# Kernel tuning notes

Hardware: AMD Instinct MI355X
Metric: run time of the kernel (lower is better)

Reference implementation:

```python
import jax, jax.numpy as jnp
import numpy as np

T, B, OBS, H, P, L, A = 512, 128, 512, 256, 128, 4, 4


def _ln(x, scale, bias, eps=1e-6):
    mu = jnp.mean(x, axis=-1, keepdims=True)
    var = jnp.mean((x - mu) ** 2, axis=-1, keepdims=True)
    return (x - mu) * jax.lax.rsqrt(var + eps) * scale + bias


def _binop(qi, qj):
    # S5 reset-aware associative operator: elements (A, b, reset_flag)
    Ai, bi, ci = qi
    Aj, bj, cj = qj
    A = (Aj * Ai) * (1.0 - cj) + Aj * cj
    b = (Aj * bi + bj) * (1.0 - cj) + bj * cj
    c = ci * (1.0 - cj) + cj
    return A, b, c


def _s5_layer(x, dones, h0, scale, bias, lam_re, lam_im, b_re, b_im, c_re, c_im, d_vec, log_step, glu_W, glu_b):
    # x: (T,B,H) real, dones: (T,B), h0: (B,P) complex64
    skip = x
    u = _ln(x, scale, bias)                                  # prenorm
    lam = lam_re + 1j * lam_im                               # (P,)
    step = jnp.exp(log_step)                                 # (P,)
    lam_bar = jnp.exp(lam * step)                            # ZOH discretization
    B_bar = ((lam_bar - 1.0) / lam)[:, None] * (b_re + 1j * b_im)  # (P,H)
    Bu = jnp.einsum('tbh,ph->tbp', u.astype(jnp.complex64), B_bar)  # (T,B,P)
    A_el = jnp.concatenate([jnp.ones((1, B, P), jnp.complex64),
                            jnp.broadcast_to(lam_bar.astype(jnp.complex64), (T, B, P))], axis=0)
    b_el = jnp.concatenate([h0[None], Bu], axis=0)
    c_el = jnp.concatenate([jnp.zeros((1, B, 1), jnp.float32), dones[..., None]], axis=0)
    _, xs, _ = jax.lax.associative_scan(_binop, (A_el, b_el, c_el), axis=0)
    xs = xs[1:]                                              # (T,B,P) complex states
    new_h = xs[-1]
    C = c_re + 1j * c_im                                     # (H,P)
    ys = 2.0 * jnp.real(jnp.einsum('tbp,hp->tbh', xs, C)) + d_vec * u  # conj_sym output + D*u
    z = _ln(ys, scale, bias)                                 # gtrxl norm (shared LayerNorm params)
    z = jax.nn.gelu(z)                                       # half_glu1
    z = z * jax.nn.sigmoid(z @ glu_W + glu_b)
    return skip + z, new_h


def setup_inputs() -> dict:
    key = jax.random.key(0)
    ks = jax.random.split(key, 40)
    f32 = jnp.float32

    def n(i, shape, s=1.0):
        return jax.random.normal(ks[i], shape, f32) * s

    inp = {}
    inp['obs'] = n(0, (T, B, OBS))
    inp['dones'] = (jax.random.uniform(ks[1], (T, B)) < 0.01).astype(f32)
    inp['hidden_re'] = jnp.zeros((L, B, P), f32)
    inp['hidden_im'] = jnp.zeros((L, B, P), f32)
    inp['enc0_W'] = n(2, (OBS, 128), 1.0 / np.sqrt(OBS))
    inp['enc0_b'] = jnp.zeros((128,), f32)
    inp['enc1_W'] = n(3, (128, H), 1.0 / np.sqrt(128))
    inp['enc1_b'] = jnp.zeros((H,), f32)
    inp['norm_scale'] = jnp.ones((L, H), f32)
    inp['norm_bias'] = jnp.zeros((L, H), f32)
    inp['Lambda_re'] = -0.5 * jax.random.uniform(ks[4], (L, P), f32) - 0.1
    inp['Lambda_im'] = n(5, (L, P), np.pi)
    inp['B_re'] = n(6, (L, P, H), 1.0 / np.sqrt(H))
    inp['B_im'] = n(7, (L, P, H), 1.0 / np.sqrt(H))
    inp['C_re'] = n(8, (L, H, P), 1.0 / np.sqrt(2 * P))
    inp['C_im'] = n(9, (L, H, P), 1.0 / np.sqrt(2 * P))
    inp['D'] = n(10, (L, H))
    inp['log_step'] = jax.random.uniform(ks[11], (L, P), f32, np.log(1e-3), np.log(1e-1))
    inp['glu_W'] = n(12, (L, H, H), 1.0 / np.sqrt(H))
    inp['glu_b'] = jnp.zeros((L, H), f32)
    inp['ab0_W'] = n(13, (H, 128), 1.0 / np.sqrt(H))
    inp['ab0_b'] = jnp.zeros((128,), f32)
    inp['ab1_W'] = n(14, (128, 128), 1.0 / np.sqrt(128))
    inp['ab1_b'] = jnp.zeros((128,), f32)
    inp['adec_W'] = n(15, (128, A), 0.01 / np.sqrt(128))
    inp['adec_b'] = jnp.full((A,), 0.5, f32)
    inp['log_std'] = jnp.full((A,), -0.7, f32)
    inp['vb0_W'] = n(16, (H, 128), 1.0 / np.sqrt(H))
    inp['vb0_b'] = jnp.zeros((128,), f32)
    inp['vb1_W'] = n(17, (128, 128), 1.0 / np.sqrt(128))
    inp['vb1_b'] = jnp.zeros((128,), f32)
    inp['vdec_W'] = n(18, (128, 1), 1.0 / np.sqrt(128))
    inp['vdec_b'] = jnp.zeros((1,), f32)
    return inp


def reference(obs, dones, hidden_re, hidden_im, enc0_W, enc0_b, enc1_W, enc1_b,
              norm_scale, norm_bias, Lambda_re, Lambda_im, B_re, B_im, C_re, C_im,
              D, log_step, glu_W, glu_b, ab0_W, ab0_b, ab1_W, ab1_b, adec_W, adec_b,
              log_std, vb0_W, vb0_b, vb1_W, vb1_b, vdec_W, vdec_b):
    e = jax.nn.leaky_relu(obs @ enc0_W + enc0_b)
    e = jax.nn.leaky_relu(e @ enc1_W + enc1_b)
    h0 = (hidden_re + 1j * hidden_im).astype(jnp.complex64)  # (L,B,P)
    new_h = []
    for l in range(L):
        e, hl = _s5_layer(e, dones, h0[l], norm_scale[l], norm_bias[l],
                          Lambda_re[l], Lambda_im[l], B_re[l], B_im[l],
                          C_re[l], C_im[l], D[l], log_step[l], glu_W[l], glu_b[l])
        new_h.append(hl)
    new_h = jnp.stack(new_h)
    am = jax.nn.leaky_relu(e @ ab0_W + ab0_b)
    am = jax.nn.leaky_relu(am @ ab1_W + ab1_b)
    am = am @ adec_W + adec_b                                # actor mean (T,B,A)
    v = jax.nn.leaky_relu(e @ vb0_W + vb0_b)
    v = jax.nn.leaky_relu(v @ vb1_W + vb1_b)
    v = v @ vdec_W + vdec_b                                  # critic (T,B,1)
    sc = jnp.broadcast_to(jnp.exp(log_std), am.shape)        # Normal scale (pi params)
    out = jnp.concatenate([am, sc, v], axis=-1)              # (T,B,2A+1)
    return out, jnp.real(new_h), jnp.imag(new_h)
```

## Files before the change

kernel.cpp:

```cpp
#include <hip/hip_runtime.h>
#include <math.h>

#define TT 512
#define BB 128
#define OBSD 512
#define HD 256
#define PD 128
#define LD 4
#define NTB (TT*BB)

typedef __bf16 bf16x8 __attribute__((ext_vector_type(8)));
typedef float  f32x4  __attribute__((ext_vector_type(4)));

__device__ __forceinline__ float bf2f(unsigned short u) {
    return __uint_as_float(((unsigned)u) << 16);
}
__device__ __forceinline__ unsigned short f2bf(float f) {
    unsigned u = __float_as_uint(f);
    unsigned r = (u + 0x7FFFu + ((u >> 16) & 1u)) >> 16;
    return (unsigned short)r;
}
__device__ __forceinline__ float gelu_f(float x) {
    float x3 = x * x * x;
    return 0.5f * x * (1.f + tanhf(0.7978845608028654f * (x + 0.044715f * x3)));
}


template<int LAST>
__global__ __launch_bounds__(512) void layer_k(
    const unsigned short* __restrict__ XSp,
    const unsigned short* __restrict__ Uaux,
    const unsigned short* __restrict__ CT,
    const unsigned short* __restrict__ GT,
    const unsigned short* __restrict__ BT2,
    const float* __restrict__ Dv,
    const float* __restrict__ ns1, const float* __restrict__ nb1,
    const float* __restrict__ glub,
    const float* __restrict__ ns2, const float* __restrict__ nb2,
    unsigned short* __restrict__ Xio,
    unsigned short* __restrict__ Uo,
    unsigned short* __restrict__ BUo)
{
    const int N = 256;
    __shared__ unsigned short smA[2 * 2048];
    __shared__ unsigned short smB[2 * 8192];
    __shared__ unsigned short zbuf[64 * 264];
    float2 (*red)[8] = reinterpret_cast<float2(*)[8]>(&smA[0]);
    int tid = threadIdx.x;
    int lane = tid & 63, w = tid >> 6;
    int m16 = lane & 15, quad = lane >> 4;
    int m0 = blockIdx.x * 64;
    int colb = w * 32 + quad * 4;

    auto stage1 = [&](int slot, int kt) {
        int k0 = kt << 5;
#pragma unroll
        for (int j = 0; j < 2; ++j) {
            int e = (w * 2 + j) * 128 + lane * 2;
            int row = e >> 5, kb = e & 31;
            const unsigned short* g = XSp + (size_t)(m0 + row) * 256 + k0 + kb;
            __builtin_amdgcn_global_load_lds(
                (const __attribute__((address_space(1))) void*)g,
                (__attribute__((address_space(3))) void*)(smA + slot * 2048 + e), 4, 0, 0);
        }
#pragma unroll
        for (int j = 0; j < 2; ++j) {
            int e = (w * 2 + j) * 512 + lane * 8;
            int r = e >> 5, kq = e & 31;
            const unsigned short* g = CT + (size_t)r * 256 + k0 + kq;
            __builtin_amdgcn_global_load_lds(
                (const __attribute__((address_space(1))) void*)g,
                (__attribute__((address_space(3))) void*)(smB + slot * 8192 + e), 16, 0, 0);
        }
    };
    auto stageB = [&](const unsigned short* BT, int slot, int kt) {
        int k0 = kt << 5;
#pragma unroll
        for (int j = 0; j < 2; ++j) {
            int e = (w * 2 + j) * 512 + lane * 8;
            int r = e >> 5, kq = e & 31;
            const unsigned short* g = BT + (size_t)r * 256 + k0 + kq;
            __builtin_amdgcn_global_load_lds(
                (const __attribute__((address_space(1))) void*)g,
                (__attribute__((address_space(3))) void*)(smB + slot * 8192 + e), 16, 0, 0);
        }
    };

    f32x4 acc[4][2] = {};
    stage1(0, 0);
    for (int t = 0; t < 8; ++t) {
        int cur = t & 1;
        if (t + 1 < 8) {
            stage1(cur ^ 1, t + 1);
            asm volatile("s_waitcnt vmcnt(4)" ::: "memory");
        } else {
            asm volatile("s_waitcnt vmcnt(0)" ::: "memory");
        }
        __builtin_amdgcn_s_barrier();
        __builtin_amdgcn_sched_barrier(0);
        bf16x8 af[4], bfr[2];
#pragma unroll
        for (int mi = 0; mi < 4; ++mi)
            af[mi] = *(const bf16x8*)(smA + cur * 2048 + (mi * 16 + m16) * 32 + quad * 8);
#pragma unroll
        for (int nj = 0; nj < 2; ++nj)
            bfr[nj] = *(const bf16x8*)(smB + cur * 8192 + (w * 2 + nj) * 512 + m16 * 32 + quad * 8);
#pragma unroll
        for (int mi = 0; mi < 4; ++mi)
#pragma unroll
            for (int nj = 0; nj < 2; ++nj)
                acc[mi][nj] = __builtin_amdgcn_mfma_f32_16x16x32_bf16(
                    bfr[nj], af[mi], acc[mi][nj], 0, 0, 0);
        __builtin_amdgcn_sched_barrier(0);
        __builtin_amdgcn_s_barrier();
    }

    stageB(GT, 0, 0);

#pragma unroll
    for (int mi = 0; mi < 4; ++mi) {
        int row_l = mi * 16 + m16;
        size_t rowb = (size_t)(m0 + row_l) * N;
        float s = 0.f, q = 0.f;
#pragma unroll
        for (int nj = 0; nj < 2; ++nj) {
            float4 dn = *(const float4*)(Dv + colb + nj * 16);
            ushort4 a1 = *(const ushort4*)(Uaux + rowb + colb + nj * 16);
#pragma unroll
            for (int r = 0; r < 4; ++r) {
                float d = (r == 0) ? dn.x : (r == 1) ? dn.y : (r == 2) ? dn.z : dn.w;
                float u = bf2f(r == 0 ? a1.x : r == 1 ? a1.y : r == 2 ? a1.z : a1.w);
                float v = acc[mi][nj][r] + d * u;
                acc[mi][nj][r] = v;
                s += v; q += v * v;
            }
        }
        s += __shfl_xor(s, 16); q += __shfl_xor(q, 16);
        s += __shfl_xor(s, 32); q += __shfl_xor(q, 32);
        if (quad == 0) red[row_l][w] = float2{s, q};
    }
    __syncthreads();
#pragma unroll
    for (int mi = 0; mi < 4; ++mi) {
        int row_l = mi * 16 + m16;
        float S = 0.f, Q = 0.f;
#pragma unroll
        for (int ww = 0; ww < 8; ++ww) { float2 tv = red[row_l][ww]; S += tv.x; Q += tv.y; }
        float mu = S * (1.f / 256.f);
        float var = Q * (1.f / 256.f) - mu * mu;
        float rstd = rsqrtf(var + 1e-6f);
#pragma unroll
        for (int nj = 0; nj < 2; ++nj) {
            float4 ls = *(const float4*)(ns1 + colb + nj * 16);
            float4 lb = *(const float4*)(nb1 + colb + nj * 16);
            float o[4];
#pragma unroll
            for (int r = 0; r < 4; ++r) {
                float sc = (r == 0) ? ls.x : (r == 1) ? ls.y : (r == 2) ? ls.z : ls.w;
                float bi = (r == 0) ? lb.x : (r == 1) ? lb.y : (r == 2) ? lb.z : lb.w;
                o[r] = gelu_f((acc[mi][nj][r] - mu) * rstd * sc + bi);
            }
            ushort4 ov = { f2bf(o[0]), f2bf(o[1]), f2bf(o[2]), f2bf(o[3]) };
            *(ushort4*)(zbuf + row_l * 264 + colb + nj * 16) = ov;
        }
    }
    __syncthreads();

    f32x4 acc2[4][2] = {};
    for (int t = 0; t < 8; ++t) {
        int cur = t & 1;
        if (t + 1 < 8) {
            stageB(GT, cur ^ 1, t + 1);
            asm volatile("s_waitcnt vmcnt(2)" ::: "memory");
        } else {
            asm volatile("s_waitcnt vmcnt(0)" ::: "memory");
        }
        __builtin_amdgcn_s_barrier();
        __builtin_amdgcn_sched_barrier(0);
        bf16x8 af[4], bfr[2];
#pragma unroll
        for (int mi = 0; mi < 4; ++mi)
            af[mi] = *(const bf16x8*)(zbuf + (mi * 16 + m16) * 264 + t * 32 + quad * 8);
#pragma unroll
        for (int nj = 0; nj < 2; ++nj)
            bfr[nj] = *(const bf16x8*)(smB + cur * 8192 + (w * 2 + nj) * 512 + m16 * 32 + quad * 8);
#pragma unroll
        for (int mi = 0; mi < 4; ++mi)
#pragma unroll
            for (int nj = 0; nj < 2; ++nj)
                acc2[mi][nj] = __builtin_amdgcn_mfma_f32_16x16x32_bf16(
                    bfr[nj], af[mi], acc2[mi][nj], 0, 0, 0);
        __builtin_amdgcn_sched_barrier(0);
        __builtin_amdgcn_s_barrier();
    }

    if (!LAST) stageB(BT2, 0, 0);

#pragma unroll
    for (int mi = 0; mi < 4; ++mi) {
        int row_l = mi * 16 + m16;
        size_t rowb = (size_t)(m0 + row_l) * N;
        float s = 0.f, q = 0.f;
#pragma unroll
        for (int nj = 0; nj < 2; ++nj) {
            float4 gb = *(const float4*)(glub + colb + nj * 16);
            ushort4 zz = *(const ushort4*)(zbuf + row_l * 264 + colb + nj * 16);
            ushort4 xo = *(const ushort4*)(Xio + rowb + colb + nj * 16);
            float vv[4];
#pragma unroll
            for (int r = 0; r < 4; ++r) {
                float bv = (r == 0) ? gb.x : (r == 1) ? gb.y : (r == 2) ? gb.z : gb.w;
                float zv = bf2f(r == 0 ? zz.x : r == 1 ? zz.y : r == 2 ? zz.z : zz.w);
                float xv = bf2f(r == 0 ? xo.x : r == 1 ? xo.y : r == 2 ? xo.z : xo.w);
                float sg = 1.f / (1.f + expf(-(acc2[mi][nj][r] + bv)));
                float v = xv + zv * sg;
                vv[r] = v;
                acc2[mi][nj][r] = v;
                s += v; q += v * v;
            }
            ushort4 o = { f2bf(vv[0]), f2bf(vv[1]), f2bf(vv[2]), f2bf(vv[3]) };
            *(ushort4*)(Xio + rowb + colb + nj * 16) = o;
        }
        if (!LAST) {
            s += __shfl_xor(s, 16); q += __shfl_xor(q, 16);
            s += __shfl_xor(s, 32); q += __shfl_xor(q, 32);
            if (quad == 0) red[row_l][w] = float2{s, q};
        }
    }
    if (LAST) return;
    __syncthreads();

#pragma unroll
    for (int mi = 0; mi < 4; ++mi) {
        int row_l = mi * 16 + m16;
        float S = 0.f, Q = 0.f;
#pragma unroll
        for (int ww = 0; ww < 8; ++ww) { float2 tv = red[row_l][ww]; S += tv.x; Q += tv.y; }
        float mu = S * (1.f / 256.f);
        float var = Q * (1.f / 256.f) - mu * mu;
        float rstd = rsqrtf(var + 1e-6f);
        size_t rowb = (size_t)(m0 + row_l) * N;
#pragma unroll
        for (int nj = 0; nj < 2; ++nj) {
            float4 ls = *(const float4*)(ns2 + colb + nj * 16);
            float4 lb = *(const float4*)(nb2 + colb + nj * 16);
            float o[4];
#pragma unroll
            for (int r = 0; r < 4; ++r) {
                float sc = (r == 0) ? ls.x : (r == 1) ? ls.y : (r == 2) ? ls.z : ls.w;
                float bi = (r == 0) ? lb.x : (r == 1) ? lb.y : (r == 2) ? lb.z : lb.w;
                o[r] = (acc2[mi][nj][r] - mu) * rstd * sc + bi;
            }
            ushort4 ov = { f2bf(o[0]), f2bf(o[1]), f2bf(o[2]), f2bf(o[3]) };
            *(ushort4*)(Uo + rowb + colb + nj * 16) = ov;
            *(ushort4*)(zbuf + row_l * 264 + colb + nj * 16) = ov;
        }
    }
    __syncthreads();

    f32x4 acc3[4][2] = {};
    for (int t = 0; t < 8; ++t) {
        int cur = t & 1;
        if (t + 1 < 8) {
            stageB(BT2, cur ^ 1, t + 1);
            asm volatile("s_waitcnt vmcnt(2)" ::: "memory");
        } else {
            asm volatile("s_waitcnt vmcnt(0)" ::: "memory");
        }
        __builtin_amdgcn_s_barrier();
        __builtin_amdgcn_sched_barrier(0);
        bf16x8 af[4], bfr[2];
#pragma unroll
        for (int mi = 0; mi < 4; ++mi)
            af[mi] = *(const bf16x8*)(zbuf + (mi * 16 + m16) * 264 + t * 32 + quad * 8);
#pragma unroll
        for (int nj = 0; nj < 2; ++nj)
            bfr[nj] = *(const bf16x8*)(smB + cur * 8192 + (w * 2 + nj) * 512 + m16 * 32 + quad * 8);
#pragma unroll
        for (int mi = 0; mi < 4; ++mi)
#pragma unroll
            for (int nj = 0; nj < 2; ++nj)
                acc3[mi][nj] = __builtin_amdgcn_mfma_f32_16x16x32_bf16(
                    bfr[nj], af[mi], acc3[mi][nj], 0, 0, 0);
        __builtin_amdgcn_sched_barrier(0);
        __builtin_amdgcn_s_barrier();
    }
#pragma unroll
    for (int mi = 0; mi < 4; ++mi) {
        size_t rowb = (size_t)(m0 + mi * 16 + m16) * N;
#pragma unroll
        for (int nj = 0; nj < 2; ++nj) {
            ushort4 o = { f2bf(acc3[mi][nj][0]), f2bf(acc3[mi][nj][1]),
                          f2bf(acc3[mi][nj][2]), f2bf(acc3[mi][nj][3]) };
            *(ushort4*)(BUo + rowb + colb + nj * 16) = o;
        }
    }
}

__global__ __launch_bounds__(512) void enc1_bu_k(
    const unsigned short* __restrict__ U1p,
    const unsigned short* __restrict__ E1T,
    const unsigned short* __restrict__ BT0,
    const float* __restrict__ e1b,
    const float* __restrict__ ns0, const float* __restrict__ nb0,
    unsigned short* __restrict__ Xio,
    unsigned short* __restrict__ Uo,
    unsigned short* __restrict__ BUo)
{
    const int N = 256;
    __shared__ unsigned short smA[2 * 2048];
    __shared__ unsigned short smB[2 * 8192];
    __shared__ unsigned short zbuf[64 * 264];
    float2 (*red)[8] = reinterpret_cast<float2(*)[8]>(&smA[0]);
    int tid = threadIdx.x;
    int lane = tid & 63, w = tid >> 6;
    int m16 = lane & 15, quad = lane >> 4;
    int m0 = blockIdx.x * 64;
    int colb = w * 32 + quad * 4;

    auto stage1 = [&](int slot, int kt) {
        int k0 = kt << 5;
#pragma unroll
        for (int j = 0; j < 2; ++j) {
            int e = (w * 2 + j) * 128 + lane * 2;
            int row = e >> 5, kb = e & 31;
            const unsigned short* g = U1p + (size_t)(m0 + row) * 128 + k0 + kb;
            __builtin_amdgcn_global_load_lds(
                (const __attribute__((address_space(1))) void*)g,
                (__attribute__((address_space(3))) void*)(smA + slot * 2048 + e), 4, 0, 0);
        }
#pragma unroll
        for (int j = 0; j < 2; ++j) {
            int e = (w * 2 + j) * 512 + lane * 8;
            int r = e >> 5, kq = e & 31;
            const unsigned short* g = E1T + (size_t)r * 128 + k0 + kq;
            __builtin_amdgcn_global_load_lds(
                (const __attribute__((address_space(1))) void*)g,
                (__attribute__((address_space(3))) void*)(smB + slot * 8192 + e), 16, 0, 0);
        }
    };
    auto stageB = [&](int slot, int kt) {
        int k0 = kt << 5;
#pragma unroll
        for (int j = 0; j < 2; ++j) {
            int e = (w * 2 + j) * 512 + lane * 8;
            int r = e >> 5, kq = e & 31;
// ... 28 lines not shown
#pragma unroll
            for (int nj = 0; nj < 2; ++nj)
                acc[mi][nj] = __builtin_amdgcn_mfma_f32_16x16x32_bf16(
                    bfr[nj], af[mi], acc[mi][nj], 0, 0, 0);
        __builtin_amdgcn_sched_barrier(0);
        __builtin_amdgcn_s_barrier();
    }

    stageB(0, 0);

#pragma unroll
    for (int mi = 0; mi < 4; ++mi) {
        int row_l = mi * 16 + m16;
        size_t rowb = (size_t)(m0 + row_l) * N;
        float s = 0.f, q = 0.f;
#pragma unroll
        for (int nj = 0; nj < 2; ++nj) {
            float4 bn = *(const float4*)(e1b + colb + nj * 16);
            float vv[4];
#pragma unroll
            for (int r = 0; r < 4; ++r) {
                float v = acc[mi][nj][r];
                float bv = (r == 0) ? bn.x : (r == 1) ? bn.y : (r == 2) ? bn.z : bn.w;
                v += bv; v = v > 0.f ? v : 0.01f * v;
                vv[r] = v;
                acc[mi][nj][r] = v;
                s += v; q += v * v;
            }
            ushort4 o = { f2bf(vv[0]), f2bf(vv[1]), f2bf(vv[2]), f2bf(vv[3]) };
            *(ushort4*)(Xio + rowb + colb + nj * 16) = o;
        }
        s += __shfl_xor(s, 16); q += __shfl_xor(q, 16);
        s += __shfl_xor(s, 32); q += __shfl_xor(q, 32);
        if (quad == 0) red[row_l][w] = float2{s, q};
    }
    __syncthreads();
#pragma unroll
    for (int mi = 0; mi < 4; ++mi) {
        int row_l = mi * 16 + m16;
        float S = 0.f, Q = 0.f;
#pragma unroll
        for (int ww = 0; ww < 8; ++ww) { float2 tv = red[row_l][ww]; S += tv.x; Q += tv.y; }
        float mu = S * (1.f / 256.f);
        float var = Q * (1.f / 256.f) - mu * mu;
        float rstd = rsqrtf(var + 1e-6f);
        size_t rowb = (size_t)(m0 + row_l) * N;
#pragma unroll
        for (int nj = 0; nj < 2; ++nj) {
            float4 ls = *(const float4*)(ns0 + colb + nj * 16);
            float4 lb = *(const float4*)(nb0 + colb + nj * 16);
            float o[4];
#pragma unroll
            for (int r = 0; r < 4; ++r) {
                float sc = (r == 0) ? ls.x : (r == 1) ? ls.y : (r == 2) ? ls.z : ls.w;
                float bi = (r == 0) ? lb.x : (r == 1) ? lb.y : (r == 2) ? lb.z : lb.w;
                o[r] = (acc[mi][nj][r] - mu) * rstd * sc + bi;
            }
            ushort4 ov = { f2bf(o[0]), f2bf(o[1]), f2bf(o[2]), f2bf(o[3]) };
            *(ushort4*)(Uo + rowb + colb + nj * 16) = ov;
            *(ushort4*)(zbuf + row_l * 264 + colb + nj * 16) = ov;
        }
    }
    __syncthreads();

    f32x4 acc2[4][2] = {};
    for (int t = 0; t < 8; ++t) {
        int cur = t & 1;
        if (t + 1 < 8) {
            stageB(cur ^ 1, t + 1);
            asm volatile("s_waitcnt vmcnt(2)" ::: "memory");
        } else {
            asm volatile("s_waitcnt vmcnt(0)" ::: "memory");
        }
        __builtin_amdgcn_s_barrier();
        __builtin_amdgcn_sched_barrier(0);
// ... 8 lines not shown
        for (int mi = 0; mi < 4; ++mi)
#pragma unroll
            for (int nj = 0; nj < 2; ++nj)
                acc2[mi][nj] = __builtin_amdgcn_mfma_f32_16x16x32_bf16(
                    bfr[nj], af[mi], acc2[mi][nj], 0, 0, 0);
        __builtin_amdgcn_sched_barrier(0);
        __builtin_amdgcn_s_barrier();
    }
#pragma unroll
    for (int mi = 0; mi < 4; ++mi) {
        size_t rowb = (size_t)(m0 + mi * 16 + m16) * N;
#pragma unroll
        for (int nj = 0; nj < 2; ++nj) {
            ushort4 o = { f2bf(acc2[mi][nj][0]), f2bf(acc2[mi][nj][1]),
                          f2bf(acc2[mi][nj][2]), f2bf(acc2[mi][nj][3]) };
            *(ushort4*)(BUo + rowb + colb + nj * 16) = o;
        }
    }
}

__global__ __launch_bounds__(512) void head_fused_k(
    const unsigned short* __restrict__ Xp, const unsigned short* __restrict__ W0T,
    const float* __restrict__ cb0,
    const unsigned short* __restrict__ AB1T, const unsigned short* __restrict__ VB1T,
    const float* __restrict__ ab1b, const float* __restrict__ vb1b,
    const float* __restrict__ adW, const float* __restrict__ adb,
    const float* __restrict__ lstd,
    const float* __restrict__ vdW, const float* __restrict__ vdb,
    float* __restrict__ out)
{
    __shared__ unsigned short smA[2 * 2048];
    __shared__ unsigned short smB[2 * 8192];
    __shared__ unsigned short zbuf[64 * 264];
    float (*redh)[8][4] = reinterpret_cast<float(*)[8][4]>(&smA[0]);
    int tid = threadIdx.x;
    int lane = tid & 63, w = tid >> 6;
    int m16 = lane & 15, quad = lane >> 4;
    int m0 = blockIdx.x * 64;
    int colb = w * 32 + quad * 4;

    f32x4 acc[4][2] = {};

    auto stage1 = [&](int slot, int kt) {
        int k0 = kt << 5;
#pragma unroll
        for (int j = 0; j < 2; ++j) {
            int e = (w * 2 + j) * 128 + lane * 2;
            int row = e >> 5, kb = e & 31;
            const unsigned short* g = Xp + (size_t)(m0 + row) * 256 + k0 + kb;
            __builtin_amdgcn_global_load_lds(
                (const __attribute__((address_space(1))) void*)g,
                (__attribute__((address_space(3))) void*)(smA + slot * 2048 + e), 4, 0, 0);
        }
#pragma unroll
        for (int j = 0; j < 2; ++j) {
            int e = (w * 2 + j) * 512 + lane * 8;
            int p = e >> 11, r = (e >> 5) & 63, kq = e & 31;
            const unsigned short* g = W0T + (size_t)(p * 64 + r) * 256 + k0 + kq;
            __builtin_amdgcn_global_load_lds(
                (const __attribute__((address_space(1))) void*)g,
                (__attribute__((address_space(3))) void*)(smB + slot * 8192 + e), 16, 0, 0);
        }
    };
    auto stage2 = [&](int slot, int kt) {
        int k0 = kt << 5;
#pragma unroll
        for (int j = 0; j < 2; ++j) {
            int e = (w * 2 + j) * 512 + lane * 8;
            int r = e >> 5, kq = e & 31;
            const unsigned short* g = (r < 128)
                ? AB1T + (size_t)r * 128 + k0 + kq
                : VB1T + (size_t)(r - 128) * 128 + k0 + kq;
            __builtin_amdgcn_global_load_lds(
                (const __attribute__((address_space(1))) void*)g,
                (__attribute__((address_space(3))) void*)(smB + slot * 8192 + e), 16, 0, 0);
        }
    };

    stage1(0, 0);
    for (int t = 0; t < 8; ++t) {
        int cur = t & 1;
        if (t + 1 < 8) {
            stage1(cur ^ 1, t + 1);
            asm volatile("s_waitcnt vmcnt(4)" ::: "memory");
        } else {
            asm volatile("s_waitcnt vmcnt(0)" ::: "memory");
        }
        __builtin_amdgcn_s_barrier();
        __builtin_amdgcn_sched_barrier(0);
        bf16x8 af[4], bfr[2];
#pragma unroll
// ... 61 lines not shown

    float pd[4][4] = {};
    float pv[4] = {0.f, 0.f, 0.f, 0.f};
#pragma unroll
    for (int nj = 0; nj < 2; ++nj)
#pragma unroll
        for (int r = 0; r < 4; ++r) {
            int c = (w & 3) * 32 + nj * 16 + quad * 4 + r;
            float bb = (w < 4) ? ab1b[c] : vb1b[c];
            float4 aw = {0.f, 0.f, 0.f, 0.f};
            float vw = 0.f;
            if (w < 4) aw = *(const float4*)(adW + c * 4);
            else       vw = vdW[c];
#pragma unroll
            for (int mi = 0; mi < 4; ++mi) {
                float v = acc2[mi][nj][r] + bb;
                v = v > 0.f ? v : 0.01f * v;
                if (w < 4) {
                    pd[mi][0] += v * aw.x; pd[mi][1] += v * aw.y;
                    pd[mi][2] += v * aw.z; pd[mi][3] += v * aw.w;
                } else {
                    pv[mi] += v * vw;
                }
            }
        }
#pragma unroll
    for (int mi = 0; mi < 4; ++mi) {
        int row_l = mi * 16 + m16;
        if (w < 4) {
#pragma unroll
            for (int a = 0; a < 4; ++a) {
                float x = pd[mi][a];
                x += __shfl_xor(x, 16); x += __shfl_xor(x, 32);
                if (quad == 0) redh[row_l][w][a] = x;
            }
        } else {
            float x = pv[mi];
            x += __shfl_xor(x, 16); x += __shfl_xor(x, 32);
            if (quad == 0) redh[row_l][w][0] = x;
        }
    }
    __syncthreads();
    if (tid < 64) {
        size_t o = (size_t)(m0 + tid) * 9;
#pragma unroll
        for (int a = 0; a < 4; ++a)
            out[o + a] = redh[tid][0][a] + redh[tid][1][a] + redh[tid][2][a] + redh[tid][3][a] + adb[a];
#pragma unroll
        for (int a = 0; a < 4; ++a) out[o + 4 + a] = expf(lstd[a]);
        out[o + 8] = redh[tid][4][0] + redh[tid][5][0] + redh[tid][6][0] + redh[tid][7][0] + vdb[0];
    }
}

__global__ __launch_bounds__(256) void mgemm_obs(
    const float* __restrict__ A, const unsigned short* __restrict__ BT,
    unsigned short* __restrict__ U, const float* __restrict__ bias)
{
    const int K = 512, NJ = 2, N = 128;
    __shared__ unsigned short smA[64 * 32];
    __shared__ unsigned short smB[NJ * 64 * 32];
    int tid = threadIdx.x;
    int lane = tid & 63, w = tid >> 6;
    int m16 = lane & 15, quad = lane >> 4;
    int m0 = blockIdx.x * 64;

    f32x4 acc[4][NJ] = {};
    for (int k0 = 0; k0 < K; k0 += 32) {
#pragma unroll
        for (int p = 0; p < 2; ++p) {
            int idx = p * 256 + tid;
            int r = idx >> 3, kq = (idx & 7) * 4;
            float4 v = *(const float4*)(A + (size_t)(m0 + r) * K + k0 + kq);
            ushort4 o = { f2bf(v.x), f2bf(v.y), f2bf(v.z), f2bf(v.w) };
            *(ushort4*)(smA + r * 32 + kq) = o;
        }
#pragma unroll
        for (int p = 0; p < NJ; ++p) {
            const unsigned short* g = BT + (size_t)(p * 64 + (tid >> 2)) * K + k0 + (tid & 3) * 8;
            unsigned short* l = smB + p * 2048 + tid * 8;
            __builtin_amdgcn_global_load_lds(
                (const __attribute__((address_space(1))) void*)g,
                (__attribute__((address_space(3))) void*)l, 16, 0, 0);
        }
        __syncthreads();
        bf16x8 af[4], bfr[NJ];
#pragma unroll
        for (int mi = 0; mi < 4; ++mi)
            af[mi] = *(const bf16x8*)(smA + (mi * 16 + m16) * 32 + quad * 8);
#pragma unroll
        for (int nj = 0; nj < NJ; ++nj)
            bfr[nj] = *(const bf16x8*)(smB + (w * NJ * 16 + nj * 16 + m16) * 32 + quad * 8);
#pragma unroll
        for (int mi = 0; mi < 4; ++mi)
#pragma unroll
            for (int nj = 0; nj < NJ; ++nj)
                acc[mi][nj] = __builtin_amdgcn_mfma_f32_16x16x32_bf16(
                    bfr[nj], af[mi], acc[mi][nj], 0, 0, 0);
        __syncthreads();
    }
    int colb = w * NJ * 16 + quad * 4;
#pragma unroll
    for (int mi = 0; mi < 4; ++mi) {
        size_t rowb = (size_t)(m0 + mi * 16 + m16) * N;
#pragma unroll
        for (int nj = 0; nj < NJ; ++nj) {
            float4 bv = *(const float4*)(bias + colb + nj * 16);
            float v0 = acc[mi][nj][0] + bv.x; v0 = v0 > 0.f ? v0 : 0.01f * v0;
            float v1 = acc[mi][nj][1] + bv.y; v1 = v1 > 0.f ? v1 : 0.01f * v1;
            float v2 = acc[mi][nj][2] + bv.z; v2 = v2 > 0.f ? v2 : 0.01f * v2;
            float v3 = acc[mi][nj][3] + bv.w; v3 = v3 > 0.f ? v3 : 0.01f * v3;
            ushort4 o = { f2bf(v0), f2bf(v1), f2bf(v2), f2bf(v3) };
            *(ushort4*)(U + rowb + colb + nj * 16) = o;
        }
    }
}

__global__ __launch_bounds__(512) void scan2_k(
    const unsigned short* __restrict__ bu, unsigned short* __restrict__ xs,
    const float* __restrict__ dones,
    const float* __restrict__ h0re, const float* __restrict__ h0im,
    const float* __restrict__ lamre, const float* __restrict__ lamim,
    const float* __restrict__ lstep,
    float* __restrict__ outre, float* __restrict__ outim)
{
    __shared__ float sdone[TT];
    __shared__ float4 ssum[16][32];
    __shared__ float2 shin[16][32];
    int tid = threadIdx.x;
    int b  = blockIdx.x >> 2;
    int ph = blockIdx.x & 3;
    int chunk = tid >> 5, pl = tid & 31;
// ... 164 lines not shown
    unsigned short* BU    = (unsigned short*)(wsb + 160 * MB);
    char* wgt = wsb + 192 * MB;
    unsigned short* BBART = (unsigned short*)(wgt);
    unsigned short* CCATT = (unsigned short*)(wgt + 512 * 1024);
    unsigned short* GLUT  = (unsigned short*)(wgt + 1024 * 1024);
    unsigned short* E0T   = (unsigned short*)(wgt + 1536 * 1024);
    unsigned short* E1T   = (unsigned short*)(wgt + 1664 * 1024);
    unsigned short* AB0VT = (unsigned short*)(wgt + 1728 * 1024);
    unsigned short* AB1T  = (unsigned short*)(wgt + 1856 * 1024);
    unsigned short* VB1T  = (unsigned short*)(wgt + 1888 * 1024);
    float*          CB0   = (float*)(wgt + 1920 * 1024);

    float* out   = (float*)d_out;
    float* outre = out + (size_t)NTB * 9;
    float* outim = outre + LD * BB * PD;

    prep_k<<<512, 256, 0, stream>>>(B_re, B_im, C_re, C_im, Lre, Lim, lstep, BBART, CCATT);
    tcvt_k<<<256, 256, 0, stream>>>(enc0_W, E0T, 512, 128);
    tcvt_k<<<128, 256, 0, stream>>>(enc1_W, E1T, 128, 256);
    tcvt4_k<<<1024, 256, 0, stream>>>(glu_W, GLUT);
    tcvt_k<<<128, 256, 0, stream>>>(ab0_W, AB0VT, 256, 128);
    tcvt_k<<<128, 256, 0, stream>>>(vb0_W, AB0VT + 128 * 256, 256, 128);
    tcvt_k<<<64, 256, 0, stream>>>(ab1_W, AB1T, 128, 128);
    tcvt_k<<<64, 256, 0, stream>>>(vb1_W, VB1T, 128, 128);
    catb_k<<<1, 256, 0, stream>>>(ab0_b, vb0_b, CB0);

    mgemm_obs<<<1024, 256, 0, stream>>>(obs, E0T, U1, enc0_b);
    enc1_bu_k<<<1024, 512, 0, stream>>>(U1, E1T, BBART, enc1_b, nsc, nbi, X, U, BU);

    for (int l = 0; l < LD; ++l) {
        scan2_k<<<512, 512, 0, stream>>>(BU, XS, dones, hre + l * BB * PD, him + l * BB * PD,
                                         Lre + l * PD, Lim + l * PD, lstep + l * PD,
                                         outre + l * BB * PD, outim + l * BB * PD);
        if (l + 1 < LD) {
            layer_k<0><<<1024, 512, 0, stream>>>(XS, U,
                CCATT + (size_t)l * 65536, GLUT + (size_t)l * 65536,
                BBART + (size_t)(l + 1) * 65536,
                Dv + l * HD, nsc + l * HD, nbi + l * HD, glu_b + l * HD,
                nsc + (l + 1) * HD, nbi + (l + 1) * HD, X, U, BU);
        } else {
            layer_k<1><<<1024, 512, 0, stream>>>(XS, U,
                CCATT + (size_t)l * 65536, GLUT + (size_t)l * 65536, nullptr,
                Dv + l * HD, nsc + l * HD, nbi + l * HD, glu_b + l * HD,
                nullptr, nullptr, X, nullptr, nullptr);
        }
    }

    head_fused_k<<<1024, 512, 0, stream>>>(X, AB0VT, CB0, AB1T, VB1T, ab1_b, vb1_b,
                                           adec_W, adec_b, log_std, vdec_W, vdec_b, out);
}
```

Measured before the change: 927.0 us.

## Split fused S5 layer kernel and pipeline GEMM loads with deeper buffering

Measured after the change: 872.6 us. 5.9% less time.

```diff
diff --git a/kernel.cpp b/kernel.cpp
--- a/kernel.cpp
+++ b/kernel.cpp
@@ -25,16 +25,167 @@
     return 0.5f * x * (1.f + tanhf(0.7978845608028654f * (x + 0.044715f * x3)));
 }
 
-
-template<int LAST>
-__global__ __launch_bounds__(512) void layer_k(
-    const unsigned short* __restrict__ XSp,
-    const unsigned short* __restrict__ Uaux,
-    const unsigned short* __restrict__ CT,
+template<int MODE, int NJ, int NK>
+__global__ __launch_bounds__(512) void mgemm2(
+    const unsigned short* __restrict__ A, const unsigned short* __restrict__ BT,
+    int LDA, const float* __restrict__ bias,
+    const float* __restrict__ lnsc, const float* __restrict__ lnbi,
+    const unsigned short* __restrict__ aux1, unsigned short* Xio,
+    unsigned short* __restrict__ U, int wU)
+{
+    constexpr int NJW = NJ / 2;
+    constexpr int LPS = 2 + NJW;
+    constexpr int K = NK * 32;
+    const int N = NJ * 64;
+    __shared__ unsigned short smA[3 * 2048];
+    __shared__ unsigned short smB[3 * NJ * 2048];
+    float2 (*red)[64] = reinterpret_cast<float2(*)[64]>(&smA[0]);
+    int tid = threadIdx.x;
+    int lane = tid & 63, w = tid >> 6;
+    int m16 = lane & 15, quad = lane >> 4;
+    int m0 = blockIdx.x * 64;
+
+    f32x4 acc[4][NJW] = {};
+
+    auto stage = [&](int slot, int kt) {
+        int k0 = kt << 5;
+#pragma unroll
+        for (int j = 0; j < 2; ++j) {
+            int chunk = w * 2 + j;
+            int e = chunk * 128 + lane * 2;
+            int row = e >> 5, kb = e & 31;
+            const unsigned short* g = A + (size_t)(m0 + row) * LDA + k0 + kb;
+            __builtin_amdgcn_global_load_lds(
+                (const __attribute__((address_space(1))) void*)g,
+                (__attribute__((address_space(3))) void*)(smA + slot * 2048 + e), 4, 0, 0);
+        }
+#pragma unroll
+        for (int j = 0; j < NJW; ++j) {
+            int chunk = w * NJW + j;
+            int e = chunk * 512 + lane * 8;
+            int p = e >> 11, r = (e >> 5) & 63, kq = e & 31;
+            const unsigned short* g = BT + (size_t)(p * 64 + r) * K + k0 + kq;
+            __builtin_amdgcn_global_load_lds(
+                (const __attribute__((address_space(1))) void*)g,
+                (__attribute__((address_space(3))) void*)(smB + slot * NJ * 2048 + e), 16, 0, 0);
+        }
+    };
+
+    int nk = NK;
+    stage(0, 0);
+    stage(1, 1);
+    int cur = 0, nxt = 2;
+    for (int t = 0; t < nk; ++t) {
+        int rem = nk - 1 - t;
+        if (rem >= 2) {
+            stage(nxt, t + 2);
+            nxt = (nxt == 2) ? 0 : nxt + 1;
+            asm volatile("s_waitcnt vmcnt(%0)" :: "i"(2 * LPS) : "memory");
+        } else if (rem == 1) {
+            asm volatile("s_waitcnt vmcnt(%0)" :: "i"(LPS) : "memory");
+        } else {
+            asm volatile("s_waitcnt vmcnt(0)" ::: "memory");
+        }
+        __builtin_amdgcn_s_barrier();
+        __builtin_amdgcn_sched_barrier(0);
+        bf16x8 af[4], bfr[NJW];
+#pragma unroll
+        for (int mi = 0; mi < 4; ++mi)
+            af[mi] = *(const bf16x8*)(smA + cur * 2048 + (mi * 16 + m16) * 32 + quad * 8);
+#pragma unroll
+        for (int nj = 0; nj < NJW; ++nj)
+            bfr[nj] = *(const bf16x8*)(smB + cur * NJ * 2048 + (w * NJW + nj) * 512 + m16 * 32 + quad * 8);
+#pragma unroll
+        for (int mi = 0; mi < 4; ++mi)
+#pragma unroll
+            for (int nj = 0; nj < NJW; ++nj)
+                acc[mi][nj] = __builtin_amdgcn_mfma_f32_16x16x32_bf16(
+                    bfr[nj], af[mi], acc[mi][nj], 0, 0, 0);
+        __builtin_amdgcn_sched_barrier(0);
+        __builtin_amdgcn_s_barrier();
+        cur = (cur == 2) ? 0 : cur + 1;
+    }
+
+    int colb = w * (NJW * 16) + quad * 4;
+
+#pragma unroll
+    for (int mi = 0; mi < 4; ++mi) {
+        size_t rowb = (size_t)(m0 + mi * 16 + m16) * N;
+        float s = 0.f, q = 0.f;
+#pragma unroll
+        for (int nj = 0; nj < NJW; ++nj) {
+            float4 bn = *(const float4*)(bias + colb + nj * 16);
+            ushort4 a1, xo;
+            a1 = *(const ushort4*)(aux1 + rowb + colb + nj * 16);
+            if (MODE == 3) xo = *(const ushort4*)(Xio + rowb + colb + nj * 16);
+            float vv[4];
+#pragma unroll
+            for (int r = 0; r < 4; ++r) {
+                float v = acc[mi][nj][r];
+                float bv = (r == 0) ? bn.x : (r == 1) ? bn.y : (r == 2) ? bn.z : bn.w;
+                if (MODE == 2) {
+                    float u = bf2f(r == 0 ? a1.x : r == 1 ? a1.y : r == 2 ? a1.z : a1.w);
+                    v += bv * u;
+                } else {
+                    float zz = bf2f(r == 0 ? a1.x : r == 1 ? a1.y : r == 2 ? a1.z : a1.w);
+                    float xx = bf2f(r == 0 ? xo.x : r == 1 ? xo.y : r == 2 ? xo.z : xo.w);
+                    float sg = 1.f / (1.f + expf(-(v + bv)));
+                    v = xx + zz * sg;
+                }
+                vv[r] = v;
+                acc[mi][nj][r] = v;
+                s += v; q += v * v;
+            }
+            if (MODE == 3) {
+                ushort4 o = { f2bf(vv[0]), f2bf(vv[1]), f2bf(vv[2]), f2bf(vv[3]) };
+                *(ushort4*)(Xio + rowb + colb + nj * 16) = o;
+            }
+        }
+        if (MODE != 3 || wU) {
+            s += __shfl_xor(s, 16); q += __shfl_xor(q, 16);
+            s += __shfl_xor(s, 32); q += __shfl_xor(q, 32);
+            if (quad == 0) red[w][mi * 16 + m16] = float2{s, q};
+        }
+    }
+    if (MODE == 3 && !wU) return;
+    __syncthreads();
+
+#pragma unroll
+    for (int mi = 0; mi < 4; ++mi) {
+        int row_l = mi * 16 + m16;
+        float S = 0.f, Q = 0.f;
+#pragma unroll
+        for (int ww = 0; ww < 8; ++ww) {
+            float2 tv = red[ww][row_l];
+            S += tv.x; Q += tv.y;
+        }
+        float mu = S * (1.f / 256.f);
+        float var = Q * (1.f / 256.f) - mu * mu;
+        float rstd = rsqrtf(var + 1e-6f);
+        size_t rowb = (size_t)(m0 + row_l) * N;
+#pragma unroll
+        for (int nj = 0; nj < NJW; ++nj) {
+            float4 ls = *(const float4*)(lnsc + colb + nj * 16);
+            float4 lb = *(const float4*)(lnbi + colb + nj * 16);
+            float o[4];
+#pragma unroll
+            for (int r = 0; r < 4; ++r) {
+                float sc = (r == 0) ? ls.x : (r == 1) ? ls.y : (r == 2) ? ls.z : ls.w;
+                float bi = (r == 0) ? lb.x : (r == 1) ? lb.y : (r == 2) ? lb.z : lb.w;
+                float v = (acc[mi][nj][r] - mu) * rstd * sc + bi;
+                if (MODE == 2) v = gelu_f(v);
+                o[r] = v;
+            }
+            ushort4 ov = { f2bf(o[0]), f2bf(o[1]), f2bf(o[2]), f2bf(o[3]) };
+            *(ushort4*)(U + rowb + colb + nj * 16) = ov;
+        }
+    }
+}
+
+__global__ __launch_bounds__(512) void glu_bu_k(
+    const unsigned short* __restrict__ Z,
     const unsigned short* __restrict__ GT,
     const unsigned short* __restrict__ BT2,
-    const float* __restrict__ Dv,
-    const float* __restrict__ ns1, const float* __restrict__ nb1,
     const float* __restrict__ glub,
     const float* __restrict__ ns2, const float* __restrict__ nb2,
     unsigned short* __restrict__ Xio,
@@ -45,20 +196,22 @@
     __shared__ unsigned short smA[2 * 2048];
     __shared__ unsigned short smB[2 * 8192];
     __shared__ unsigned short zbuf[64 * 264];
-    float2 (*red)[8] = reinterpret_cast<float2(*)[8]>(&smA[0]);
+    float2 (*red)[64] = reinterpret_cast<float2(*)[64]>(&smA[0]);
     int tid = threadIdx.x;
     int lane = tid & 63, w = tid >> 6;
     int m16 = lane & 15, quad = lane >> 4;
     int m0 = blockIdx.x * 64;
     int colb = w * 32 + quad * 4;
 
+    f32x4 acc[4][2] = {};
+
     auto stage1 = [&](int slot, int kt) {
         int k0 = kt << 5;
 #pragma unroll
         for (int j = 0; j < 2; ++j) {
             int e = (w * 2 + j) * 128 + lane * 2;
             int row = e >> 5, kb = e & 31;
-            const unsigned short* g = XSp + (size_t)(m0 + row) * 256 + k0 + kb;
+            const unsigned short* g = Z + (size_t)(m0 + row) * 256 + k0 + kb;
             __builtin_amdgcn_global_load_lds(
                 (const __attribute__((address_space(1))) void*)g,
                 (__attribute__((address_space(3))) void*)(smA + slot * 2048 + e), 4, 0, 0);
@@ -67,7 +220,7 @@
         for (int j = 0; j < 2; ++j) {
             int e = (w * 2 + j) * 512 + lane * 8;
             int r = e >> 5, kq = e & 31;
-            const unsigned short* g = CT + (size_t)r * 256 + k0 + kq;
+            const unsigned short* g = GT + (size_t)r * 256 + k0 + kq;
             __builtin_amdgcn_global_load_lds(
                 (const __attribute__((address_space(1))) void*)g,
                 (__attribute__((address_space(3))) void*)(smB + slot * 8192 + e), 16, 0, 0);
@@ -86,7 +239,6 @@
         }
     };
 
-    f32x4 acc[4][2] = {};
     stage1(0, 0);
     for (int t = 0; t < 8; ++t) {
         int cur = t & 1;
@@ -115,7 +267,7 @@
         __builtin_amdgcn_s_barrier();
     }
 
-    stageB(GT, 0, 0);
+    stageB(BT2, 0, 0);
 
 #pragma unroll
     for (int mi = 0; mi < 4; ++mi) {
@@ -124,110 +276,29 @@
         float s = 0.f, q = 0.f;
 #pragma unroll
         for (int nj = 0; nj < 2; ++nj) {
-            float4 dn = *(const float4*)(Dv + colb + nj * 16);
-            ushort4 a1 = *(const ushort4*)(Uaux + rowb + colb + nj * 16);
-#pragma unroll
-            for (int r = 0; r < 4; ++r) {
-                float d = (r == 0) ? dn.x : (r == 1) ? dn.y : (r == 2) ? dn.z : dn.w;
-                float u = bf2f(r == 0 ? a1.x : r == 1 ? a1.y : r == 2 ? a1.z : a1.w);
-                float v = acc[mi][nj][r] + d * u;
-                acc[mi][nj][r] = v;
-                s += v; q += v * v;
-            }
-        }
-        s += __shfl_xor(s, 16); q += __shfl_xor(q, 16);
-        s += __shfl_xor(s, 32); q += __shfl_xor(q, 32);
-        if (quad == 0) red[row_l][w] = float2{s, q};
-    }
-    __syncthreads();
-#pragma unroll
-    for (int mi = 0; mi < 4; ++mi) {
-        int row_l = mi * 16 + m16;
-        float S = 0.f, Q = 0.f;
-#pragma unroll
-        for (int ww = 0; ww < 8; ++ww) { float2 tv = red[row_l][ww]; S += tv.x; Q += tv.y; }
-        float mu = S * (1.f / 256.f);
-        float var = Q * (1.f / 256.f) - mu * mu;
-        float rstd = rsqrtf(var + 1e-6f);
-#pragma unroll
-        for (int nj = 0; nj < 2; ++nj) {
-            float4 ls = *(const float4*)(ns1 + colb + nj * 16);
-            float4 lb = *(const float4*)(nb1 + colb + nj * 16);
-            float o[4];
-#pragma unroll
-            for (int r = 0; r < 4; ++r) {
-                float sc = (r == 0) ? ls.x : (r == 1) ? ls.y : (r == 2) ? ls.z : ls.w;
-                float bi = (r == 0) ? lb.x : (r == 1) ? lb.y : (r == 2) ? lb.z : lb.w;
-                o[r] = gelu_f((acc[mi][nj][r] - mu) * rstd * sc + bi);
-            }
-            ushort4 ov = { f2bf(o[0]), f2bf(o[1]), f2bf(o[2]), f2bf(o[3]) };
-            *(ushort4*)(zbuf + row_l * 264 + colb + nj * 16) = ov;
-        }
-    }
-    __syncthreads();
-
-    f32x4 acc2[4][2] = {};
-    for (int t = 0; t < 8; ++t) {
-        int cur = t & 1;
-        if (t + 1 < 8) {
-            stageB(GT, cur ^ 1, t + 1);
-            asm volatile("s_waitcnt vmcnt(2)" ::: "memory");
-        } else {
-            asm volatile("s_waitcnt vmcnt(0)" ::: "memory");
-        }
-        __builtin_amdgcn_s_barrier();
-        __builtin_amdgcn_sched_barrier(0);
-        bf16x8 af[4], bfr[2];
-#pragma unroll
-        for (int mi = 0; mi < 4; ++mi)
-            af[mi] = *(const bf16x8*)(zbuf + (mi * 16 + m16) * 264 + t * 32 + quad * 8);
-#pragma unroll
-        for (int nj = 0; nj < 2; ++nj)
-            bfr[nj] = *(const bf16x8*)(smB + cur * 8192 + (w * 2 + nj) * 512 + m16 * 32 + quad * 8);
-#pragma unroll
-        for (int mi = 0; mi < 4; ++mi)
-#pragma unroll
-            for (int nj = 0; nj < 2; ++nj)
-                acc2[mi][nj] = __builtin_amdgcn_mfma_f32_16x16x32_bf16(
-                    bfr[nj], af[mi], acc2[mi][nj], 0, 0, 0);
-        __builtin_amdgcn_sched_barrier(0);
-        __builtin_amdgcn_s_barrier();
-    }
-
-    if (!LAST) stageB(BT2, 0, 0);
-
-#pragma unroll
-    for (int mi = 0; mi < 4; ++mi) {
-        int row_l = mi * 16 + m16;
-        size_t rowb = (size_t)(m0 + row_l) * N;
-        float s = 0.f, q = 0.f;
-#pragma unroll
-        for (int nj = 0; nj < 2; ++nj) {
             float4 gb = *(const float4*)(glub + colb + nj * 16);
-            ushort4 zz = *(const ushort4*)(zbuf + row_l * 264 + colb + nj * 16);
+            ushort4 a1 = *(const ushort4*)(Z + rowb + colb + nj * 16);
             ushort4 xo = *(const ushort4*)(Xio + rowb + colb + nj * 16);
             float vv[4];
 #pragma unroll
             for (int r = 0; r < 4; ++r) {
+                float v = acc[mi][nj][r];
                 float bv = (r == 0) ? gb.x : (r == 1) ? gb.y : (r == 2) ? gb.z : gb.w;
-                float zv = bf2f(r == 0 ? zz.x : r == 1 ? zz.y : r == 2 ? zz.z : zz.w);
-                float xv = bf2f(r == 0 ? xo.x : r == 1 ? xo.y : r == 2 ? xo.z : xo.w);
-                float sg = 1.f / (1.f + expf(-(acc2[mi][nj][r] + bv)));
-                float v = xv + zv * sg;
+                float zz = bf2f(r == 0 ? a1.x : r == 1 ? a1.y : r == 2 ? a1.z : a1.w);
+                float xx = bf2f(r == 0 ? xo.x : r == 1 ? xo.y : r == 2 ? xo.z : xo.w);
+                float sg = 1.f / (1.f + expf(-(v + bv)));
+                v = xx + zz * sg;
                 vv[r] = v;
-                acc2[mi][nj][r] = v;
+                acc[mi][nj][r] = v;
                 s += v; q += v * v;
             }
             ushort4 o = { f2bf(vv[0]), f2bf(vv[1]), f2bf(vv[2]), f2bf(vv[3]) };
             *(ushort4*)(Xio + rowb + colb + nj * 16) = o;
         }
-        if (!LAST) {
-            s += __shfl_xor(s, 16); q += __shfl_xor(q, 16);
-            s += __shfl_xor(s, 32); q += __shfl_xor(q, 32);
-            if (quad == 0) red[row_l][w] = float2{s, q};
-        }
-    }
-    if (LAST) return;
+        s += __shfl_xor(s, 16); q += __shfl_xor(q, 16);
+        s += __shfl_xor(s, 32); q += __shfl_xor(q, 32);
+        if (quad == 0) red[w][row_l] = float2{s, q};
+    }
     __syncthreads();
 
 #pragma unroll
@@ -235,7 +306,7 @@
         int row_l = mi * 16 + m16;
         float S = 0.f, Q = 0.f;
 #pragma unroll
-        for (int ww = 0; ww < 8; ++ww) { float2 tv = red[row_l][ww]; S += tv.x; Q += tv.y; }
+        for (int ww = 0; ww < 8; ++ww) { float2 tv = red[ww][row_l]; S += tv.x; Q += tv.y; }
         float mu = S * (1.f / 256.f);
         float var = Q * (1.f / 256.f) - mu * mu;
         float rstd = rsqrtf(var + 1e-6f);
@@ -249,7 +320,7 @@
             for (int r = 0; r < 4; ++r) {
                 float sc = (r == 0) ? ls.x : (r == 1) ? ls.y : (r == 2) ? ls.z : ls.w;
                 float bi = (r == 0) ? lb.x : (r == 1) ? lb.y : (r == 2) ? lb.z : lb.w;
-                o[r] = (acc2[mi][nj][r] - mu) * rstd * sc + bi;
+                o[r] = (acc[mi][nj][r] - mu) * rstd * sc + bi;
             }
             ushort4 ov = { f2bf(o[0]), f2bf(o[1]), f2bf(o[2]), f2bf(o[3]) };
             *(ushort4*)(Uo + rowb + colb + nj * 16) = ov;
@@ -258,7 +329,7 @@
     }
     __syncthreads();
 
-    f32x4 acc3[4][2] = {};
+    f32x4 acc2[4][2] = {};
     for (int t = 0; t < 8; ++t) {
         int cur = t & 1;
         if (t + 1 < 8) {
@@ -280,8 +351,8 @@
         for (int mi = 0; mi < 4; ++mi)
 #pragma unroll
             for (int nj = 0; nj < 2; ++nj)
-                acc3[mi][nj] = __builtin_amdgcn_mfma_f32_16x16x32_bf16(
-                    bfr[nj], af[mi], acc3[mi][nj], 0, 0, 0);
+                acc2[mi][nj] = __builtin_amdgcn_mfma_f32_16x16x32_bf16(
+                    bfr[nj], af[mi], acc2[mi][nj], 0, 0, 0);
         __builtin_amdgcn_sched_barrier(0);
         __builtin_amdgcn_s_barrier();
     }
@@ -290,8 +361,8 @@
         size_t rowb = (size_t)(m0 + mi * 16 + m16) * N;
 #pragma unroll
         for (int nj = 0; nj < 2; ++nj) {
-            ushort4 o = { f2bf(acc3[mi][nj][0]), f2bf(acc3[mi][nj][1]),
-                          f2bf(acc3[mi][nj][2]), f2bf(acc3[mi][nj][3]) };
+            ushort4 o = { f2bf(acc2[mi][nj][0]), f2bf(acc2[mi][nj][1]),
+                          f2bf(acc2[mi][nj][2]), f2bf(acc2[mi][nj][3]) };
             *(ushort4*)(BUo + rowb + colb + nj * 16) = o;
         }
     }
@@ -311,7 +382,7 @@
     __shared__ unsigned short smA[2 * 2048];
     __shared__ unsigned short smB[2 * 8192];
     __shared__ unsigned short zbuf[64 * 264];
-    float2 (*red)[8] = reinterpret_cast<float2(*)[8]>(&smA[0]);
+    float2 (*red)[64] = reinterpret_cast<float2(*)[64]>(&smA[0]);
     int tid = threadIdx.x;
     int lane = tid & 63, w = tid >> 6;
     int m16 = lane & 15, quad = lane >> 4;
@@ -406,7 +477,7 @@
         }
         s += __shfl_xor(s, 16); q += __shfl_xor(q, 16);
         s += __shfl_xor(s, 32); q += __shfl_xor(q, 32);
-        if (quad == 0) red[row_l][w] = float2{s, q};
+        if (quad == 0) red[w][row_l] = float2{s, q};
     }
     __syncthreads();
 #pragma unroll
@@ -414,7 +485,7 @@
         int row_l = mi * 16 + m16;
         float S = 0.f, Q = 0.f;
 #pragma unroll
-        for (int ww = 0; ww < 8; ++ww) { float2 tv = red[row_l][ww]; S += tv.x; Q += tv.y; }
+        for (int ww = 0; ww < 8; ++ww) { float2 tv = red[ww][row_l]; S += tv.x; Q += tv.y; }
         float mu = S * (1.f / 256.f);
         float var = Q * (1.f / 256.f) - mu * mu;
         float rstd = rsqrtf(var + 1e-6f);
@@ -489,7 +560,7 @@
     __shared__ unsigned short smA[2 * 2048];
     __shared__ unsigned short smB[2 * 8192];
     __shared__ unsigned short zbuf[64 * 264];
-    float (*redh)[8][4] = reinterpret_cast<float(*)[8][4]>(&smA[0]);
+    float (*redh)[64][4] = reinterpret_cast<float(*)[64][4]>(&smA[0]);
     int tid = threadIdx.x;
     int lane = tid & 63, w = tid >> 6;
     int m16 = lane & 15, quad = lane >> 4;
@@ -512,8 +583,8 @@
 #pragma unroll
         for (int j = 0; j < 2; ++j) {
             int e = (w * 2 + j) * 512 + lane * 8;
-            int p = e >> 11, r = (e >> 5) & 63, kq = e & 31;
-            const unsigned short* g = W0T + (size_t)(p * 64 + r) * 256 + k0 + kq;
+            int r = e >> 5, kq = e & 31;
+            const unsigned short* g = W0T + (size_t)r * 256 + k0 + kq;
             __builtin_amdgcn_global_load_lds(
                 (const __attribute__((address_space(1))) void*)g,
                 (__attribute__((address_space(3))) void*)(smB + slot * 8192 + e), 16, 0, 0);
@@ -641,12 +712,12 @@
             for (int a = 0; a < 4; ++a) {
                 float x = pd[mi][a];
                 x += __shfl_xor(x, 16); x += __shfl_xor(x, 32);
-                if (quad == 0) redh[row_l][w][a] = x;
+                if (quad == 0) redh[w][row_l][a] = x;
             }
         } else {
             float x = pv[mi];
             x += __shfl_xor(x, 16); x += __shfl_xor(x, 32);
-            if (quad == 0) redh[row_l][w][0] = x;
+            if (quad == 0) redh[w][row_l][0] = x;
         }
     }
     __syncthreads();
@@ -654,10 +725,10 @@
         size_t o = (size_t)(m0 + tid) * 9;
 #pragma unroll
         for (int a = 0; a < 4; ++a)
-            out[o + a] = redh[tid][0][a] + redh[tid][1][a] + redh[tid][2][a] + redh[tid][3][a] + adb[a];
+            out[o + a] = redh[0][tid][a] + redh[1][tid][a] + redh[2][tid][a] + redh[3][tid][a] + adb[a];
 #pragma unroll
         for (int a = 0; a < 4; ++a) out[o + 4 + a] = expf(lstd[a]);
-        out[o + 8] = redh[tid][4][0] + redh[tid][5][0] + redh[tid][6][0] + redh[tid][7][0] + vdb[0];
+        out[o + 8] = redh[4][tid][0] + redh[5][tid][0] + redh[6][tid][0] + redh[7][tid][0] + vdb[0];
     }
 }
 
@@ -665,47 +736,81 @@
     const float* __restrict__ A, const unsigned short* __restrict__ BT,
     unsigned short* __restrict__ U, const float* __restrict__ bias)
 {
-    const int K = 512, NJ = 2, N = 128;
-    __shared__ unsigned short smA[64 * 32];
-    __shared__ unsigned short smB[NJ * 64 * 32];
+    const int K = 512, NJ = 2, N = 128, NK = 16;
+    __shared__ unsigned short smA[2][64 * 32];
+    __shared__ unsigned short smB[2][NJ * 64 * 32];
     int tid = threadIdx.x;
     int lane = tid & 63, w = tid >> 6;
     int m16 = lane & 15, quad = lane >> 4;
     int m0 = blockIdx.x * 64;
 
     f32x4 acc[4][NJ] = {};
-    for (int k0 = 0; k0 < K; k0 += 32) {
+
+    auto aload = [&](float4 r[2], int kt) {
+        int k0 = kt << 5;
 #pragma unroll
         for (int p = 0; p < 2; ++p) {
             int idx = p * 256 + tid;
-            int r = idx >> 3, kq = (idx & 7) * 4;
-            float4 v = *(const float4*)(A + (size_t)(m0 + r) * K + k0 + kq);
-            ushort4 o = { f2bf(v.x), f2bf(v.y), f2bf(v.z), f2bf(v.w) };
-            *(ushort4*)(smA + r * 32 + kq) = o;
-        }
+            int rr = idx >> 3, kq = (idx & 7) * 4;
+            r[p] = *(const float4*)(A + (size_t)(m0 + rr) * K + k0 + kq);
+        }
+    };
+    auto awrite = [&](const float4 r[2], int bu) {
+#pragma unroll
+        for (int p = 0; p < 2; ++p) {
+            int idx = p * 256 + tid;
+            int rr = idx >> 3, kq = (idx & 7) * 4;
+            ushort4 o = { f2bf(r[p].x), f2bf(r[p].y), f2bf(r[p].z), f2bf(r[p].w) };
+            *(ushort4*)(&smA[bu][0] + rr * 32 + kq) = o;
+        }
+    };
+    auto stageB = [&](int bu, int kt) {
+        int k0 = kt << 5;
 #pragma unroll
         for (int p = 0; p < NJ; ++p) {
             const unsigned short* g = BT + (size_t)(p * 64 + (tid >> 2)) * K + k0 + (tid & 3) * 8;
-            unsigned short* l = smB + p * 2048 + tid * 8;
-            __builtin_amdgcn_global_load_lds(
-                (const __attribute__((address_space(1))) void*)g,
-                (__attribute__((address_space(3))) void*)l, 16, 0, 0);
-        }
-        __syncthreads();
+            __builtin_amdgcn_global_load_lds(
+                (const __attribute__((address_space(1))) void*)g,
+                (__attribute__((address_space(3))) void*)(&smB[bu][0] + p * 2048 + tid * 8), 16, 0, 0);
+        }
+    };
+
+    float4 ar[2];
+    aload(ar, 0);
+    stageB(0, 0);
+    asm volatile("s_waitcnt vmcnt(2)" ::: "memory");
+    awrite(ar, 0);
+    for (int t = 0; t < NK; ++t) {
+        int cur = t & 1;
+        float4 an[2];
+        if (t + 1 < NK) {
+            aload(an, t + 1);
+            stageB(cur ^ 1, t + 1);
+            asm volatile("s_waitcnt vmcnt(4) lgkmcnt(0)" ::: "memory");
+        } else {
+            asm volatile("s_waitcnt vmcnt(0) lgkmcnt(0)" ::: "memory");
+        }
+        __builtin_amdgcn_s_barrier();
+        __builtin_amdgcn_sched_barrier(0);
         bf16x8 af[4], bfr[NJ];
 #pragma unroll
         for (int mi = 0; mi < 4; ++mi)
-            af[mi] = *(const bf16x8*)(smA + (mi * 16 + m16) * 32 + quad * 8);
+            af[mi] = *(const bf16x8*)(&smA[cur][0] + (mi * 16 + m16) * 32 + quad * 8);
 #pragma unroll
         for (int nj = 0; nj < NJ; ++nj)
-            bfr[nj] = *(const bf16x8*)(smB + (w * NJ * 16 + nj * 16 + m16) * 32 + quad * 8);
+            bfr[nj] = *(const bf16x8*)(&smB[cur][0] + (w * NJ * 16 + nj * 16 + m16) * 32 + quad * 8);
 #pragma unroll
         for (int mi = 0; mi < 4; ++mi)
 #pragma unroll
             for (int nj = 0; nj < NJ; ++nj)
                 acc[mi][nj] = __builtin_amdgcn_mfma_f32_16x16x32_bf16(
                     bfr[nj], af[mi], acc[mi][nj], 0, 0, 0);
-        __syncthreads();
+        __builtin_amdgcn_sched_barrier(0);
+        __builtin_amdgcn_s_barrier();
+        if (t + 1 < NK) {
+            asm volatile("s_waitcnt vmcnt(2)" ::: "memory");
+            awrite(an, cur ^ 1);
+        }
     }
     int colb = w * NJ * 16 + quad * 4;
 #pragma unroll
@@ -936,17 +1041,17 @@
         scan2_k<<<512, 512, 0, stream>>>(BU, XS, dones, hre + l * BB * PD, him + l * BB * PD,
                                          Lre + l * PD, Lim + l * PD, lstep + l * PD,
                                          outre + l * BB * PD, outim + l * BB * PD);
+        mgemm2<2, 4, 8><<<1024, 512, 0, stream>>>(XS, CCATT + (size_t)l * 65536, 256,
+                                               Dv + l * HD, nsc + l * HD, nbi + l * HD, U, nullptr, U, 1);
         if (l + 1 < LD) {
-            layer_k<0><<<1024, 512, 0, stream>>>(XS, U,
-                CCATT + (size_t)l * 65536, GLUT + (size_t)l * 65536,
-                BBART + (size_t)(l + 1) * 65536,
-                Dv + l * HD, nsc + l * HD, nbi + l * HD, glu_b + l * HD,
-                nsc + (l + 1) * HD, nbi + (l + 1) * HD, X, U, BU);
+            glu_bu_k<<<1024, 512, 0, stream>>>(U, GLUT + (size_t)l * 65536,
+                                               BBART + (size_t)(l + 1) * 65536,
+                                               glu_b + l * HD,
+                                               nsc + (l + 1) * HD, nbi + (l + 1) * HD,
+                                               X, U, BU);
         } else {
-            layer_k<1><<<1024, 512, 0, stream>>>(XS, U,
-                CCATT + (size_t)l * 65536, GLUT + (size_t)l * 65536, nullptr,
-                Dv + l * HD, nsc + l * HD, nbi + l * HD, glu_b + l * HD,
-                nullptr, nullptr, X, nullptr, nullptr);
+            mgemm2<3, 4, 8><<<1024, 512, 0, stream>>>(U, GLUT + (size_t)l * 65536, 256,
+                                               glu_b + l * HD, nsc, nbi, U, X, U, 0);
         }
     }
 
```
